# Kernel tuning notes

Hardware: AMD Instinct MI355X
Metric: run time of the kernel (lower is better)

Reference implementation:

```python
import jax, jax.numpy as jnp
import numpy as np

N, D, M = 65536, 1024, 32768

def setup_inputs() -> dict:
    key = jax.random.key(0)
    k1, k2, k3, k4, k5 = jax.random.split(key, 5)
    var = jax.random.randint(k1, (N, D), -128, 128, dtype=jnp.int8)
    var_scale = jax.random.uniform(k2, (1,), jnp.float32) * 0.02 + 0.01
    indices = jax.random.randint(k3, (M, D), 0, N, dtype=jnp.int32)
    updates = (jax.random.normal(k4, (M, D)) ).astype(jnp.float16)
    smooth_scales = (jax.random.uniform(k5, (D,)) + 0.5).astype(jnp.float16)
    return {"var": var, "var_scale": var_scale, "indices": indices,
            "updates": updates, "smooth_scales": smooth_scales}

def reference(var, var_scale, indices, updates, smooth_scales):
    # dequantize int8 var with fp32 scale
    out = var.astype(jnp.float32) * var_scale  # [N, D]
    # smooth-scale the updates, promote to fp32
    upd = (updates * smooth_scales).astype(jnp.float32)  # [M, D]
    # torch scatter_add_ along axis 0: out[indices[i,j], j] += upd[i,j]
    cols = jnp.arange(out.shape[1])[None, :]  # [1, D] broadcasts vs [M, D] indices
    out = out.at[indices, cols].add(upd)
    # global abs-max -> dynamic requantization to int8
    max_val = jnp.max(jnp.abs(out))
    new_scale = max_val / 127.0
    y = jnp.clip(jnp.round(out / new_scale), -128, 127).astype(jnp.int8)
    return (y, out, new_scale[None])
```

## Files before the change

### kernel.cpp

```cpp
#include <hip/hip_runtime.h>
#include <hip/hip_fp16.h>

#define N_ROWS 65536
#define D_COLS 1024
#define M_ROWS 32768
#define QROWS  16384

using u32 = unsigned int;
using u16 = unsigned short;
typedef float f32x4 __attribute__((ext_vector_type(4)));
typedef int   i32x4 __attribute__((ext_vector_type(4)));

__global__ void init_ws_k(u32* ws) {
    if (threadIdx.x == 0 && blockIdx.x == 0) ws[0] = 0u;
}

__global__ __launch_bounds__(256) void t_idx_upd_k(const int* __restrict__ idx,
                                                   const float* __restrict__ upd,
                                                   const float* __restrict__ scl,
                                                   u16* __restrict__ idxT,
                                                   __half* __restrict__ updT) {
    __shared__ u32   sidx[64][65];
    __shared__ float supd[64][65];
    const int j0 = (int)(blockIdx.x & 15) * 64;
    const int i0 = (int)(blockIdx.x >> 4) * 64;
    const int t = threadIdx.x;

    {
        const int rr = t >> 2, c4 = t & 3;
        const int*   ip = idx + (size_t)(i0 + rr) * D_COLS + j0;
        const float* up = upd + (size_t)(i0 + rr) * D_COLS + j0;
        #pragma unroll
        for (int cq = 0; cq < 4; ++cq) {
            const int jc = cq * 16 + c4 * 4;
            const i32x4 iv = __builtin_nontemporal_load((const i32x4*)(ip + jc));
            const f32x4 uv = __builtin_nontemporal_load((const f32x4*)(up + jc));
            sidx[rr][jc] = (u32)iv.x; sidx[rr][jc+1] = (u32)iv.y;
            sidx[rr][jc+2] = (u32)iv.z; sidx[rr][jc+3] = (u32)iv.w;
            supd[rr][jc] = uv.x; supd[rr][jc+1] = uv.y;
            supd[rr][jc+2] = uv.z; supd[rr][jc+3] = uv.w;
        }
    }
    __syncthreads();

    {
        const int jj = t >> 2, seg = t & 3;
        const __half hs = __float2half(scl[j0 + jj]);
        u32 wi[8], wh[8];
        #pragma unroll
        for (int p = 0; p < 8; ++p) {
            const int r = seg * 16 + 2 * p;
            const u32 a = sidx[r][jj] & 0xffffu, b = sidx[r + 1][jj] & 0xffffu;
            wi[p] = a | (b << 16);
            const __half2 h2 = __halves2half2(__hmul(__float2half(supd[r][jj]), hs),
                                              __hmul(__float2half(supd[r + 1][jj]), hs));
            wh[p] = *reinterpret_cast<const u32*>(&h2);
        }
        u16* di = idxT + (size_t)(j0 + jj) * M_ROWS + i0 + seg * 16;
        __half* dh = updT + (size_t)(j0 + jj) * M_ROWS + i0 + seg * 16;
        ((uint4*)di)[0] = uint4{wi[0], wi[1], wi[2], wi[3]};
        ((uint4*)di)[1] = uint4{wi[4], wi[5], wi[6], wi[7]};
        ((uint4*)dh)[0] = uint4{wh[0], wh[1], wh[2], wh[3]};
        ((uint4*)dh)[1] = uint4{wh[4], wh[5], wh[6], wh[7]};
    }
}

__global__ __launch_bounds__(512) void scatter_q_k(const u16* __restrict__ idxT,
                                                   const __half* __restrict__ updT,
                                                   __half* __restrict__ sumT) {
    __shared__ float acc[QROWS];
    const int bid = (blockIdx.x & 7) * 512 + (blockIdx.x >> 3);
    const int j = bid >> 2;
    const int h = bid & 3;
    const int tid = threadIdx.x;

    float4* acc4 = (float4*)acc;
    for (int t = tid; t < QROWS / 4; t += 512) acc4[t] = float4{0.f, 0.f, 0.f, 0.f};

    const int4* ip4 = (const int4*)(idxT + (size_t)j * M_ROWS);
    const int4* up4 = (const int4*)(updT + (size_t)j * M_ROWS);
    __syncthreads();

    #pragma unroll
    for (int k = 0; k < 8; ++k) {
        const int t = k * 512 + tid;
        const int4 iv = ip4[t];
        const int4 uv = up4[t];
        const u32 iw[4] = {(u32)iv.x, (u32)iv.y, (u32)iv.z, (u32)iv.w};
        const u32 uw[4] = {(u32)uv.x, (u32)uv.y, (u32)uv.z, (u32)uv.w};
        #pragma unroll
        for (int e = 0; e < 4; ++e) {
            const int r0 = iw[e] & 0xffff, r1 = iw[e] >> 16;
            const __half2 h2 = *reinterpret_cast<const __half2*>(&uw[e]);
            if ((r0 >> 14) == h) atomicAdd(&acc[r0 & (QROWS - 1)], __half2float(__low2half(h2)));
            if ((r1 >> 14) == h) atomicAdd(&acc[r1 & (QROWS - 1)], __half2float(__high2half(h2)));
        }
    }
    __syncthreads();

    __half2* dst = (__half2*)(sumT + (size_t)j * N_ROWS + h * QROWS);
    for (int t = tid; t < QROWS / 2; t += 512)
        dst[t] = __floats2half2_rn(acc[2 * t], acc[2 * t + 1]);
}

__global__ __launch_bounds__(256) void finalize_k(const int* __restrict__ var,
                                                  const __half* __restrict__ sumT,
                                                  const float* __restrict__ var_scale,
                                                  float* __restrict__ outf,
                                                  u32* __restrict__ ws) {
    __shared__ float sm[64][65];
    __shared__ float wmax[4];
    const int r0 = (int)(blockIdx.x >> 4) * 64;
    const int j0 = (int)(blockIdx.x & 15) * 64;
    const int tid = threadIdx.x;
    const float s = var_scale[0];

    {
        const int jj = tid >> 2, seg = tid & 3;
        const __half* colp = sumT + (size_t)(j0 + jj) * N_ROWS + r0 + seg * 16;
        #pragma unroll
        for (int q = 0; q < 2; ++q) {
            const uint4 w = ((const uint4*)colp)[q];
            const u32 wv[4] = {w.x, w.y, w.z, w.w};
            #pragma unroll
            for (int i = 0; i < 4; ++i) {
                const __half2 hh = *reinterpret_cast<const __half2*>(&wv[i]);
                const float2 f = __half22float2(hh);
                const int rr = seg * 16 + q * 8 + i * 2;
                sm[rr][jj] = f.x;
                sm[rr + 1][jj] = f.y;
            }
        }
    }
    __syncthreads();

    float m = 0.f;
    #pragma unroll
    for (int k = 0; k < 4; ++k) {
        const int l = k * 256 + tid;
        const int rr = l >> 4, c4 = l & 15;
        const i32x4 v = __builtin_nontemporal_load(
            (const i32x4*)(var + (size_t)(r0 + rr) * D_COLS + j0) + c4);
        float4 o;
        o.x = (float)v.x * s + sm[rr][c4 * 4 + 0];
        o.y = (float)v.y * s + sm[rr][c4 * 4 + 1];
        o.z = (float)v.z * s + sm[rr][c4 * 4 + 2];
        o.w = (float)v.w * s + sm[rr][c4 * 4 + 3];
        ((float4*)(outf + (size_t)(r0 + rr) * D_COLS + j0))[c4] = o;
        m = fmaxf(m, fmaxf(fmaxf(fabsf(o.x), fabsf(o.y)),
                           fmaxf(fabsf(o.z), fabsf(o.w))));
    }
    for (int off = 32; off; off >>= 1) m = fmaxf(m, __shfl_xor(m, off));
    if ((tid & 63) == 0) wmax[tid >> 6] = m;
    __syncthreads();
    if (tid == 0) {
        m = fmaxf(fmaxf(wmax[0], wmax[1]), fmaxf(wmax[2], wmax[3]));
        atomicMax(ws, __float_as_uint(m));
    }
}

__global__ __launch_bounds__(256) void quant_k(const float4* __restrict__ outf4,
                                               f32x4* __restrict__ y4,
                                               const u32* __restrict__ ws,
                                               float* __restrict__ scale_out, int n4) {
    const float mx = __uint_as_float(ws[0]);
    const float inv = 127.0f / mx;
    int gid = blockIdx.x * 256 + threadIdx.x;
    if (gid == 0) scale_out[0] = mx / 127.0f;
    const int stride = gridDim.x * 256;
    for (int i = gid; i < n4; i += stride) {
        float4 v = outf4[i];
        f32x4 o;
        o.x = fminf(fmaxf(rintf(v.x * inv), -128.f), 127.f);
        o.y = fminf(fmaxf(rintf(v.y * inv), -128.f), 127.f);
        o.z = fminf(fmaxf(rintf(v.z * inv), -128.f), 127.f);
        o.w = fminf(fmaxf(rintf(v.w * inv), -128.f), 127.f);
        __builtin_nontemporal_store(o, &y4[i]);
    }
}

extern "C" void kernel_launch(void* const* d_in, const int* in_sizes, int n_in,
                              void* d_out, int out_size, void* d_ws, size_t ws_size,
                              hipStream_t stream) {
    const int*   var       = (const int*)d_in[0];
    const float* var_scale = (const float*)d_in[1];
    const int*   idx       = (const int*)d_in[2];
    const float* upd       = (const float*)d_in[3];
    const float* scl       = (const float*)d_in[4];

    float* y    = (float*)d_out;
    float* outf = y + (size_t)N_ROWS * D_COLS;
    float* scale_out = y + 2 * (size_t)N_ROWS * D_COLS;

    char* scratch = (char*)y;
    u16*    idxT = (u16*)scratch;
    __half* updT = (__half*)(scratch + (size_t)67108864);
    __half* sumT = (__half*)(scratch + (size_t)134217728);
    u32* ws = (u32*)d_ws;

    const int n4 = N_ROWS * D_COLS / 4;

    init_ws_k<<<1, 64, 0, stream>>>(ws);
    t_idx_upd_k<<<8192, 256, 0, stream>>>(idx, upd, scl, idxT, updT);
    scatter_q_k<<<4096, 512, 0, stream>>>(idxT, updT, sumT);
    finalize_k<<<16384, 256, 0, stream>>>(var, sumT, var_scale, outf, ws);
    quant_k<<<4096, 256, 0, stream>>>((const float4*)outf, (f32x4*)y, ws, scale_out, n4);
}
```

Measured before the change: 574.4 us.

## Pack index/update pairs and scatter each column once across quarter passes

The transpose kernel now packs each 16-bit index and its scaled fp16 update into one 32-bit word in a single array, in place of two separate arrays. The scatter kernel switches to one 1024-thread block per column that loads the column's packed entries into registers once. It then loops over the four row quarters in shared memory, where before four blocks each re-read the whole column. This cuts redundant global reads of the index and update data, at the cost of lower occupancy, extra barriers per quarter, and leftover dead code in the packing loop.

New measurement: 608.1 us. +5.9%, slower.

```diff
diff --git a/kernel.cpp b/kernel.cpp
--- a/kernel.cpp
+++ b/kernel.cpp
@@ -15,11 +15,10 @@
     if (threadIdx.x == 0 && blockIdx.x == 0) ws[0] = 0u;
 }
 
-__global__ __launch_bounds__(256) void t_idx_upd_k(const int* __restrict__ idx,
-                                                   const float* __restrict__ upd,
-                                                   const float* __restrict__ scl,
-                                                   u16* __restrict__ idxT,
-                                                   __half* __restrict__ updT) {
+__global__ __launch_bounds__(256) void t_pack_k(const int* __restrict__ idx,
+                                                const float* __restrict__ upd,
+                                                const float* __restrict__ scl,
+                                                u32* __restrict__ packed) {
     __shared__ u32   sidx[64][65];
     __shared__ float supd[64][65];
     const int j0 = (int)(blockIdx.x & 15) * 64;
@@ -46,61 +45,75 @@
     {
         const int jj = t >> 2, seg = t & 3;
         const __half hs = __float2half(scl[j0 + jj]);
-        u32 wi[8], wh[8];
+        u32 w[8];
         #pragma unroll
         for (int p = 0; p < 8; ++p) {
-            const int r = seg * 16 + 2 * p;
-            const u32 a = sidx[r][jj] & 0xffffu, b = sidx[r + 1][jj] & 0xffffu;
-            wi[p] = a | (b << 16);
-            const __half2 h2 = __halves2half2(__hmul(__float2half(supd[r][jj]), hs),
-                                              __hmul(__float2half(supd[r + 1][jj]), hs));
-            wh[p] = *reinterpret_cast<const u32*>(&h2);
-        }
-        u16* di = idxT + (size_t)(j0 + jj) * M_ROWS + i0 + seg * 16;
-        __half* dh = updT + (size_t)(j0 + jj) * M_ROWS + i0 + seg * 16;
-        ((uint4*)di)[0] = uint4{wi[0], wi[1], wi[2], wi[3]};
-        ((uint4*)di)[1] = uint4{wi[4], wi[5], wi[6], wi[7]};
-        ((uint4*)dh)[0] = uint4{wh[0], wh[1], wh[2], wh[3]};
-        ((uint4*)dh)[1] = uint4{wh[4], wh[5], wh[6], wh[7]};
-    }
-}
-
-__global__ __launch_bounds__(512) void scatter_q_k(const u16* __restrict__ idxT,
-                                                   const __half* __restrict__ updT,
-                                                   __half* __restrict__ sumT) {
+            const int r = seg * 8 + p;
+            const int r2 = seg * 16 + 2 * p;
+            const __half hv0 = __hmul(__float2half(supd[r2][jj]), hs);
+            const __half hv1 = __hmul(__float2half(supd[r2 + 1][jj]), hs);
+            (void)r;
+            const u32 lo = (sidx[r2][jj] & 0xffffu) |
+                           ((u32)*reinterpret_cast<const u16*>(&hv0) << 16);
+            const u32 hi = (sidx[r2 + 1][jj] & 0xffffu) |
+                           ((u32)*reinterpret_cast<const u16*>(&hv1) << 16);
+            w[p] = 0;
+            w[p] = lo;
+            ((u32*)nullptr);
+            w[p] = lo;
+            (void)hi;
+        }
+        u32 out16[16];
+        #pragma unroll
+        for (int p = 0; p < 16; ++p) {
+            const int r = seg * 16 + p;
+            const __half hv = __hmul(__float2half(supd[r][jj]), hs);
+            out16[p] = (sidx[r][jj] & 0xffffu) |
+                       ((u32)*reinterpret_cast<const u16*>(&hv) << 16);
+        }
+        u32* d = packed + (size_t)(j0 + jj) * M_ROWS + i0 + seg * 16;
+        ((uint4*)d)[0] = uint4{out16[0],  out16[1],  out16[2],  out16[3]};
+        ((uint4*)d)[1] = uint4{out16[4],  out16[5],  out16[6],  out16[7]};
+        ((uint4*)d)[2] = uint4{out16[8],  out16[9],  out16[10], out16[11]};
+        ((uint4*)d)[3] = uint4{out16[12], out16[13], out16[14], out16[15]};
+    }
+}
+
+__global__ __launch_bounds__(1024) void scatter_col_k(const u32* __restrict__ packed,
+                                                      __half* __restrict__ sumT) {
     __shared__ float acc[QROWS];
-    const int bid = (blockIdx.x & 7) * 512 + (blockIdx.x >> 3);
-    const int j = bid >> 2;
-    const int h = bid & 3;
+    const int j = (int)(blockIdx.x & 7) * 128 + (int)(blockIdx.x >> 3);
     const int tid = threadIdx.x;
 
+    const i32x4* col4 = (const i32x4*)(packed + (size_t)j * M_ROWS);
+    i32x4 v[8];
+    #pragma unroll
+    for (int k = 0; k < 8; ++k) v[k] = col4[k * 1024 + tid];
+
     float4* acc4 = (float4*)acc;
-    for (int t = tid; t < QROWS / 4; t += 512) acc4[t] = float4{0.f, 0.f, 0.f, 0.f};
-
-    const int4* ip4 = (const int4*)(idxT + (size_t)j * M_ROWS);
-    const int4* up4 = (const int4*)(updT + (size_t)j * M_ROWS);
-    __syncthreads();
-
-    #pragma unroll
-    for (int k = 0; k < 8; ++k) {
-        const int t = k * 512 + tid;
-        const int4 iv = ip4[t];
-        const int4 uv = up4[t];
-        const u32 iw[4] = {(u32)iv.x, (u32)iv.y, (u32)iv.z, (u32)iv.w};
-        const u32 uw[4] = {(u32)uv.x, (u32)uv.y, (u32)uv.z, (u32)uv.w};
-        #pragma unroll
-        for (int e = 0; e < 4; ++e) {
-            const int r0 = iw[e] & 0xffff, r1 = iw[e] >> 16;
-            const __half2 h2 = *reinterpret_cast<const __half2*>(&uw[e]);
-            if ((r0 >> 14) == h) atomicAdd(&acc[r0 & (QROWS - 1)], __half2float(__low2half(h2)));
-            if ((r1 >> 14) == h) atomicAdd(&acc[r1 & (QROWS - 1)], __half2float(__high2half(h2)));
-        }
-    }
-    __syncthreads();
-
-    __half2* dst = (__half2*)(sumT + (size_t)j * N_ROWS + h * QROWS);
-    for (int t = tid; t < QROWS / 2; t += 512)
-        dst[t] = __floats2half2_rn(acc[2 * t], acc[2 * t + 1]);
+    #pragma unroll 1
+    for (int h = 0; h < 4; ++h) {
+        for (int t = tid; t < QROWS / 4; t += 1024) acc4[t] = float4{0.f, 0.f, 0.f, 0.f};
+        __syncthreads();
+        #pragma unroll
+        for (int k = 0; k < 8; ++k) {
+            const u32 e[4] = {(u32)v[k].x, (u32)v[k].y, (u32)v[k].z, (u32)v[k].w};
+            #pragma unroll
+            for (int q = 0; q < 4; ++q) {
+                const int r = (int)(e[q] & 0xffffu);
+                if ((r >> 14) == h) {
+                    const u16 hb = (u16)(e[q] >> 16);
+                    atomicAdd(&acc[r & (QROWS - 1)],
+                              __half2float(*reinterpret_cast<const __half*>(&hb)));
+                }
+            }
+        }
+        __syncthreads();
+        __half2* dst = (__half2*)(sumT + (size_t)j * N_ROWS + h * QROWS);
+        for (int t = tid; t < QROWS / 2; t += 1024)
+            dst[t] = __floats2half2_rn(acc[2 * t], acc[2 * t + 1]);
+        __syncthreads();
+    }
 }
 
 __global__ __launch_bounds__(256) void finalize_k(const int* __restrict__ var,
@@ -193,16 +206,15 @@
     float* scale_out = y + 2 * (size_t)N_ROWS * D_COLS;
 
     char* scratch = (char*)y;
-    u16*    idxT = (u16*)scratch;
-    __half* updT = (__half*)(scratch + (size_t)67108864);
-    __half* sumT = (__half*)(scratch + (size_t)134217728);
+    u32*    packed = (u32*)scratch;
+    __half* sumT   = (__half*)(scratch + (size_t)134217728);
     u32* ws = (u32*)d_ws;
 
     const int n4 = N_ROWS * D_COLS / 4;
 
     init_ws_k<<<1, 64, 0, stream>>>(ws);
-    t_idx_upd_k<<<8192, 256, 0, stream>>>(idx, upd, scl, idxT, updT);
-    scatter_q_k<<<4096, 512, 0, stream>>>(idxT, updT, sumT);
+    t_pack_k<<<8192, 256, 0, stream>>>(idx, upd, scl, packed);
+    scatter_col_k<<<1024, 1024, 0, stream>>>(packed, sumT);
     finalize_k<<<16384, 256, 0, stream>>>(var, sumT, var_scale, outf, ws);
     quant_k<<<4096, 256, 0, stream>>>((const float4*)outf, (f32x4*)y, ws, scale_out, n4);
 }
```
